# Kernel tuning notes

Hardware: AMD Instinct MI355X
Metric: run time of the kernel (lower is better)

Reference implementation:

```python
import jax, jax.numpy as jnp
import numpy as np
from jax import lax

THRESH = 0.6      # pnet score threshold (threshold[0])
IOU_THR = 0.5     # per-scale nms threshold in detect_face
K_PICKS = 128     # fixed max number of NMS picks (jit-static)
STRIDE = 2.0
CELL = 12.0
NEG = -1e30


def _conv(x, w, b):
    y = lax.conv_general_dilated(x, w, (1, 1), 'VALID',
                                 dimension_numbers=('NCHW', 'OIHW', 'NCHW'))
    return y + b[None, :, None, None]


def _prelu(x, a):
    return jnp.where(x > 0, x, a[None, :, None, None] * x)


def _maxpool2(x):
    return lax.reduce_window(x, -jnp.inf, lax.max, (1, 1, 2, 2), (1, 1, 2, 2), 'VALID')


def _nms(boxes, scores):
    # Greedy union-IoU NMS (nms_numpy math), vectorized with a fixed pick budget.
    # boxes [N,4] (shared grid), scores [N] with invalid entries already = NEG.
    x1, y1, x2, y2 = boxes[:, 0], boxes[:, 1], boxes[:, 2], boxes[:, 3]
    area = (x2 - x1 + 1.0) * (y2 - y1 + 1.0)

    def body(live, _):
        j = jnp.argmax(live)
        s = live[j]
        ok = s > NEG * 0.5
        xx1 = jnp.maximum(x1[j], x1); yy1 = jnp.maximum(y1[j], y1)
        xx2 = jnp.minimum(x2[j], x2); yy2 = jnp.minimum(y2[j], y2)
        inter = jnp.maximum(0.0, xx2 - xx1 + 1.0) * jnp.maximum(0.0, yy2 - yy1 + 1.0)
        iou = inter / (area[j] + area - inter)
        live = jnp.where(iou > IOU_THR, NEG, live).at[j].set(NEG)
        return live, (j, ok)

    _, (idx, ok) = lax.scan(body, scores, None, length=K_PICKS)
    return idx, ok


def setup_inputs():
    key = jax.random.key(0)
    ks = jax.random.split(key, 16)
    B, H, W = 16, 384, 512
    f = lambda k, shp, s=0.1: jax.random.normal(k, shp, jnp.float32) * s
    return {
        'im_data': jax.random.uniform(ks[0], (B, 3, H, W), jnp.float32) * 255.0,
        'c1_w': f(ks[1], (10, 3, 3, 3)), 'c1_b': f(ks[2], (10,)),
        'p1': jnp.full((10,), 0.25, jnp.float32),
        'c2_w': f(ks[3], (16, 10, 3, 3)), 'c2_b': f(ks[4], (16,)),
        'p2': jnp.full((16,), 0.25, jnp.float32),
        'c3_w': f(ks[5], (32, 16, 3, 3)), 'c3_b': f(ks[6], (32,)),
        'p3': jnp.full((32,), 0.25, jnp.float32),
        'c41_w': f(ks[7], (2, 32, 1, 1)), 'c41_b': f(ks[8], (2,)),
        'c42_w': f(ks[9], (4, 32, 1, 1)), 'c42_b': f(ks[10], (4,)),
    }


def reference(im_data, c1_w, c1_b, p1, c2_w, c2_b, p2, c3_w, c3_b, p3,
              c41_w, c41_b, c42_w, c42_b):
    # --- PNet conv trunk (detect_face normalization + MTCNN PNet) ---
    x = (im_data - 127.5) * 0.0078125
    h = _prelu(_conv(x, c1_w, c1_b), p1)
    h = _maxpool2(h)                                   # 2x2 s2 (dims even -> ceil==floor)
    h = _prelu(_conv(h, c2_w, c2_b), p2)
    h = _prelu(_conv(h, c3_w, c3_b), p3)
    probs = jax.nn.softmax(_conv(h, c41_w, c41_b), axis=1)[:, 1]   # [B,Hp,Wp]
    reg = _conv(h, c42_w, c42_b)                                   # [B,4,Hp,Wp]

    # --- generateBoundingBox (dense, masked instead of nonzero; scale=1) ---
    B, Hp, Wp = probs.shape
    yy, xx = jnp.meshgrid(jnp.arange(Hp, dtype=jnp.float32),
                          jnp.arange(Wp, dtype=jnp.float32), indexing='ij')
    boxes4 = jnp.stack([jnp.floor(STRIDE * xx + 1.0).ravel(),
                        jnp.floor(STRIDE * yy + 1.0).ravel(),
                        jnp.floor(STRIDE * xx + CELL).ravel(),
                        jnp.floor(STRIDE * yy + CELL).ravel()], axis=1)  # [N,4]
    scores = probs.reshape(B, -1)                                   # [B,N]
    regf = reg.reshape(B, 4, -1).transpose(0, 2, 1)                 # [B,N,4]
    masked = jnp.where(scores >= THRESH, scores, NEG)

    # --- per-image greedy NMS (batched_nms: images independent) ---
    idx, ok = jax.vmap(_nms, in_axes=(None, 0))(boxes4, masked)     # [B,K]
    pb = boxes4[idx]                                                # [B,K,4]
    ps = jnp.take_along_axis(scores, idx, axis=1)                   # [B,K]
    pr = jnp.take_along_axis(regf, idx[..., None], axis=1)          # [B,K,4]

    w = pb[..., 2] - pb[..., 0]
    hh = pb[..., 3] - pb[..., 1]
    q1 = pb[..., 0] + pr[..., 0] * w
    q2 = pb[..., 1] + pr[..., 1] * hh
    q3 = pb[..., 2] + pr[..., 2] * w
    q4 = pb[..., 3] + pr[..., 3] * hh
    rw = q3 - q1
    rh = q4 - q2
    l = jnp.maximum(rw, rh)
    nx1 = q1 + rw * 0.5 - l * 0.5
    ny1 = q2 + rh * 0.5 - l * 0.5
    out = jnp.stack([nx1, ny1, nx1 + l, ny1 + l, ps], axis=-1)      # [B,K,5]
    return out * ok[..., None].astype(out.dtype)
```

## Files before the change

### kernel.cpp

```cpp
#include <hip/hip_runtime.h>
#include <math.h>

#define BATCH 16
#define IH 384
#define IW 512
#define C1 10
#define P1H 191
#define P1W 255
#define C2 16
#define H2 189
#define W2 253
#define C3 32
#define H3 187
#define W3 251
#define N3 (H3*W3)
#define KP 128
#define CAP 7680
#define NEGV (-1e30f)

typedef _Float16 f16x8 __attribute__((ext_vector_type(8)));
typedef _Float16 f16x4 __attribute__((ext_vector_type(4)));
typedef float    f32x16 __attribute__((ext_vector_type(16)));

#define PXT 66
#define NSUB 2

#define T1R 34
#define T1C 68
__global__ __launch_bounds__(256, 1) void k_conv1pool(
        const float* __restrict__ im, const float* __restrict__ w,
        const float* __restrict__ bia, const float* __restrict__ slope,
        float* __restrict__ outp,
        const float* __restrict__ w3, _Float16* __restrict__ wbuf) {
    __shared__ float T[3 * T1R * T1C];

    int tx = threadIdx.x, ty = threadIdx.y;
    int tid = ty * 16 + tx;
    int bx = blockIdx.x, by = blockIdx.y, bb = blockIdx.z;

    if (bx == 0 && by == 0 && bb == 0) {
        for (int e = tid; e < 4608; e += 256) {
            int oc = e / 144;
            int rem = e - oc * 144;
            int ic = rem / 9;
            int tap = rem - ic * 9;
            float v = w3[e];
            _Float16 h = (_Float16)v;
            _Float16 l = (_Float16)(v - (float)h);
            int d = ((tap * 2 + (ic >> 3)) * 32 + oc) * 8 + (ic & 7);
            wbuf[d] = h;
            wbuf[4608 + d] = l;
        }
    }

    const size_t ibase = (size_t)bb * 3 * IH * IW;
    for (int g = tid; g < 3 * T1R * 33; g += 256) {
        int ch = g / (T1R * 33);
        int rem = g - ch * (T1R * 33);
        int r = rem / 33;
        int c2 = rem - r * 33;
        int yg = 32 * by + r;
        int xg = 64 * bx + 2 * c2;
        float2 v = make_float2(0.f, 0.f);
        if (yg < IH && xg < IW)
            v = *(const float2*)(im + ibase + ((size_t)ch * IH + yg) * IW + xg);
        float2 o;
        o.x = (v.x - 127.5f) * 0.0078125f;
        o.y = (v.y - 127.5f) * 0.0078125f;
        *(float2*)&T[(ch * T1R + r) * T1C + 2 * c2] = o;
    }
    __syncthreads();

    int Y  = by * 16 + ty;
    int X0 = bx * 32 + 2 * tx;
    if (Y >= P1H) return;

    float win[3][4][6];
    #pragma unroll
    for (int ch = 0; ch < 3; ++ch)
        #pragma unroll
        for (int r = 0; r < 4; ++r) {
            const float* p = &T[(ch * T1R + 2 * ty + r) * T1C + 4 * tx];
            float4 a = *(const float4*)p;
            float2 b = *(const float2*)(p + 4);
            win[ch][r][0] = a.x; win[ch][r][1] = a.y;
            win[ch][r][2] = a.z; win[ch][r][3] = a.w;
            win[ch][r][4] = b.x; win[ch][r][5] = b.y;
        }
    #pragma unroll
    for (int ch = 0; ch < 3; ++ch)
        #pragma unroll
        for (int r = 0; r < 4; ++r)
            #pragma unroll
            for (int c = 0; c < 6; ++c)
                asm volatile("" : "+v"(win[ch][r][c]));

    bool px1ok = (X0 + 1 < P1W);
    for (int oc = 0; oc < C1; ++oc) {
        const float* wo = w + oc * 27;
        float bv = bia[oc], sv = slope[oc];
        float c0 = bv, c1 = bv, c2 = bv, c3 = bv;
        float c4 = bv, c5 = bv, c6 = bv, c7 = bv;
        #pragma unroll
        for (int ch = 0; ch < 3; ++ch)
            #pragma unroll
            for (int ky = 0; ky < 3; ++ky)
                #pragma unroll
                for (int kx = 0; kx < 3; ++kx) {
                    float wv = wo[(ch * 3 + ky) * 3 + kx];
                    c0 += win[ch][0 + ky][0 + kx] * wv;
                    c1 += win[ch][0 + ky][1 + kx] * wv;
                    c2 += win[ch][0 + ky][2 + kx] * wv;
                    c3 += win[ch][0 + ky][3 + kx] * wv;
                    c4 += win[ch][1 + ky][0 + kx] * wv;
                    c5 += win[ch][1 + ky][1 + kx] * wv;
                    c6 += win[ch][1 + ky][2 + kx] * wv;
                    c7 += win[ch][1 + ky][3 + kx] * wv;
                }
        float m0 = fmaxf(fmaxf(c0, c1), fmaxf(c4, c5));
        float m1 = fmaxf(fmaxf(c2, c3), fmaxf(c6, c7));
        float p0 = m0 > 0.f ? m0 : sv * m0;
        float p1 = m1 > 0.f ? m1 : sv * m1;
        float* o = outp + (((size_t)bb * C1 + oc) * P1H + Y) * P1W + X0;
        o[0] = p0;
        if (px1ok) o[1] = p1;
    }
}

__global__ __launch_bounds__(256, 1) void k_conv2(
        const float* __restrict__ inp, const float* __restrict__ w,
        const float* __restrict__ bia, const float* __restrict__ slope,
        float* __restrict__ outp) {
    __shared__ __align__(16) float smem[8192];
    float* tile = smem;
    float4* sbuf = (float4*)smem;

    int tx = threadIdx.x, ty = threadIdx.y;
    int tid = ty * 64 + tx;
    int bx = blockIdx.x, byb = blockIdx.y, bb = blockIdx.z;

    const float* pin = inp + (size_t)bb * C1 * P1H * P1W;
    for (int g = tid; g < C1 * 6 * 130; g += 256) {
        int ic = g / 780;
        int rem = g - ic * 780;
        int r = rem / 130;
        int c = rem - r * 130;
        int yg = 4 * byb + r;
        int xg = 128 * bx + c;
        float v = 0.f;
        if (yg < P1H && xg < P1W)
            v = pin[((size_t)ic * P1H + yg) * P1W + xg];
        tile[(ic * 6 + r) * 132 + c] = v;
    }
    __syncthreads();

    int x0 = bx * 128 + tx * 2;
    int y  = byb * 4 + ty;
    bool alive = (x0 < W2) && (y < H2);

    float a0[C2], a1[C2];
    #pragma unroll
    for (int oc = 0; oc < C2; ++oc) { a0[oc] = bia[oc]; a1[oc] = bia[oc]; }

    if (alive) {
        #pragma unroll 1
        for (int ci = 0; ci < C1; ++ci) {
            float v[3][4];
            #pragma unroll
            for (int r = 0; r < 3; ++r) {
                const float* p = &tile[(ci * 6 + ty + r) * 132 + 2 * tx];
                float2 u0 = *(const float2*)p;
                float2 u1 = *(const float2*)(p + 2);
                v[r][0] = u0.x; v[r][1] = u0.y; v[r][2] = u1.x; v[r][3] = u1.y;
            }
            #pragma unroll
            for (int r = 0; r < 3; ++r)
                #pragma unroll
                for (int k = 0; k < 4; ++k)
                    asm volatile("" : "+v"(v[r][k]));
            const float* wc = w + ci * 9;
            #pragma unroll
            for (int oc = 0; oc < C2; ++oc) {
                const float* wo = wc + oc * (C1 * 9);
                float s0 = a0[oc], s1 = a1[oc];
                #pragma unroll
                for (int ky = 0; ky < 3; ++ky)
                    #pragma unroll
                    for (int kx = 0; kx < 3; ++kx) {
                        float wv = wo[ky * 3 + kx];
                        s0 += v[ky][kx]     * wv;
                        s1 += v[ky][kx + 1] * wv;
                    }
                a0[oc] = s0; a1[oc] = s1;
            }
        }
        #pragma unroll
        for (int oc = 0; oc < C2; ++oc) {
            float sl = slope[oc];
            float u0 = a0[oc]; a0[oc] = u0 > 0.f ? u0 : sl * u0;
            float u1 = a1[oc]; a1[oc] = u1 > 0.f ? u1 : sl * u1;
        }
    }
    __syncthreads();

    #pragma unroll
    for (int c4 = 0; c4 < 4; ++c4) {
        int g0 = tid * 8 + c4;
        int p0 = g0 ^ ((g0 >> 3) & 7);
        sbuf[p0] = make_float4(a0[c4 * 4], a0[c4 * 4 + 1], a0[c4 * 4 + 2], a0[c4 * 4 + 3]);
        int g1 = tid * 8 + 4 + c4;
        int p1 = g1 ^ ((g1 >> 3) & 7);
        sbuf[p1] = make_float4(a1[c4 * 4], a1[c4 * 4 + 1], a1[c4 * 4 + 2], a1[c4 * 4 + 3]);
    }
    __syncthreads();

    const size_t obase = (size_t)bb * H2 * W2 * C2;
    #pragma unroll
    for (int it = 0; it < 8; ++it) {
        int g = it * 256 + tid;
        int c4 = g & 3, px = (g >> 2) & 127, ry = g >> 9;
        int xg = bx * 128 + px, yg = byb * 4 + ry;
        if (xg < W2 && yg < H2) {
            int phys = g ^ ((g >> 3) & 7);
            *(float4*)(outp + obase + ((size_t)yg * W2 + xg) * C2 + c4 * 4) = sbuf[phys];
        }
    }
}

__global__ __launch_bounds__(256, 2) void k_conv3mfma(
        const float* __restrict__ act,
        const _Float16* __restrict__ wbuf,
        const float* __restrict__ b3, const float* __restrict__ s3,
        const float* __restrict__ w41, const float* __restrict__ b41,
        const float* __restrict__ w42, const float* __restrict__ b42,
        float* __restrict__ scores, float4* __restrict__ regf) {
    __shared__ __align__(16) _Float16 Ah[6 * 2 * PXT * 8];
    __shared__ __align__(16) _Float16 Al[6 * 2 * PXT * 8];
    __shared__ __align__(16) float    htab[32 * 8];

    int tid = threadIdx.x;
    int bx = blockIdx.x * (NSUB * 32);
    int by = blockIdx.y * 4;
    int bb = blockIdx.z;

    {
        int oc = tid >> 3, f = tid & 7;
        float v;
        if      (f == 0) v = b3[oc];
        else if (f == 1) v = s3[oc];
        else if (f == 2) v = w41[oc];
        else if (f == 3) v = w41[32 + oc];
        else             v = w42[(f - 4) * 32 + oc];
        htab[tid] = v;
    }
    {
        const float* actb = act + (size_t)bb * H2 * W2 * C2;
        for (int e = tid; e < 6 * PXT * 4; e += 256) {
            int ic4 = e & 3;
            int t = e >> 2;
            int px = t % PXT;
            int row = t / PXT;
            int yg = by + row, xg = bx + px;
            float4 v = make_float4(0.f, 0.f, 0.f, 0.f);
            if (yg < H2 && xg < W2)
                v = *(const float4*)(actb + ((size_t)yg * W2 + xg) * C2 + ic4 * 4);
            float xs0 = v.x, xs1 = v.y, xs2 = v.z, xs3 = v.w;
            f16x4 hv, lv;
            _Float16 h;
            h = (_Float16)xs0; hv[0] = h; lv[0] = (_Float16)(xs0 - (float)h);
            h = (_Float16)xs1; hv[1] = h; lv[1] = (_Float16)(xs1 - (float)h);
            h = (_Float16)xs2; hv[2] = h; lv[2] = (_Float16)(xs2 - (float)h);
            h = (_Float16)xs3; hv[3] = h; lv[3] = (_Float16)(xs3 - (float)h);
            int kg = ic4 >> 1, h4 = ic4 & 1;
            int gr = (row * 2 + kg) * PXT + px;
            *(f16x4*)(Ah + gr * 8 + h4 * 4) = hv;
            *(f16x4*)(Al + gr * 8 + h4 * 4) = lv;
        }
    }
    __syncthreads();

    int wv = tid >> 6, lane = tid & 63;
    int col = lane & 31, half = lane >> 5;
    int y = by + wv;
    if (y >= H3) return;

    f32x16 acc[NSUB];
    #pragma unroll
    for (int s = 0; s < NSUB; ++s)
        #pragma unroll
        for (int i = 0; i < 16; ++i) acc[s][i] = 0.f;

    const _Float16* wg = wbuf + (half * 32 + col) * 8;

    #pragma unroll 1
    for (int ky = 0; ky < 3; ++ky) {
        const _Float16* arh = Ah + ((wv + ky) * 2 + half) * (PXT * 8);
        const _Float16* arl = Al + ((wv + ky) * 2 + half) * (PXT * 8);
        #pragma unroll
        for (int kx = 0; kx < 3; ++kx) {
            int tap = ky * 3 + kx;
            f16x8 wh = *(const f16x8*)(wg + tap * 512);
            f16x8 wl = *(const f16x8*)(wg + 4608 + tap * 512);
            #pragma unroll
            for (int s = 0; s < NSUB; ++s) {
                int p = s * 32 + col + kx;
                f16x8 bh = *(const f16x8*)(arh + p * 8);
                f16x8 bl = *(const f16x8*)(arl + p * 8);
                acc[s] = __builtin_amdgcn_mfma_f32_32x32x16_f16(wh, bh, acc[s], 0, 0, 0);
                acc[s] = __builtin_amdgcn_mfma_f32_32x32x16_f16(wl, bh, acc[s], 0, 0, 0);
                acc[s] = __builtin_amdgcn_mfma_f32_32x32x16_f16(wh, bl, acc[s], 0, 0, 0);
            }
        }
    }

    float L0[NSUB], L1[NSUB], R0[NSUB], R1[NSUB], R2[NSUB], R3[NSUB];
    #pragma unroll
    for (int s = 0; s < NSUB; ++s) { L0[s]=0.f; L1[s]=0.f; R0[s]=0.f; R1[s]=0.f; R2[s]=0.f; R3[s]=0.f; }

    #pragma unroll
    for (int r = 0; r < 16; ++r) {
        int oc = (r & 3) + 8 * (r >> 2) + 4 * half;
        float4 t0 = *(const float4*)&htab[oc * 8];
        float4 t1 = *(const float4*)&htab[oc * 8 + 4];
        #pragma unroll
        for (int s = 0; s < NSUB; ++s) {
            float v = acc[s][r] + t0.x;
            v = v > 0.f ? v : v * t0.y;
            L0[s] += v * t0.z; L1[s] += v * t0.w;
            R0[s] += v * t1.x; R1[s] += v * t1.y;
            R2[s] += v * t1.z; R3[s] += v * t1.w;
        }
    }

    float hb0 = b41[0], hb1 = b41[1];
    float rb0 = b42[0], rb1 = b42[1], rb2 = b42[2], rb3 = b42[3];

    #pragma unroll
    for (int s = 0; s < NSUB; ++s) {
        float l0 = L0[s] + __shfl_xor(L0[s], 32) + hb0;
        float l1 = L1[s] + __shfl_xor(L1[s], 32) + hb1;
        float r0 = R0[s] + __shfl_xor(R0[s], 32) + rb0;
        float r1 = R1[s] + __shfl_xor(R1[s], 32) + rb1;
        float r2 = R2[s] + __shfl_xor(R2[s], 32) + rb2;
        float r3 = R3[s] + __shfl_xor(R3[s], 32) + rb3;
        float m = fmaxf(l0, l1);
        float e0 = expf(l0 - m), e1 = expf(l1 - m);
        float p = e1 / (e0 + e1);
        int px = bx + s * 32 + col;
        if (half == 0 && px < W3) {
            size_t n = (size_t)bb * N3 + (size_t)y * W3 + px;
            scores[n] = (p >= 0.6f) ? p : NEGV;
            regf[n] = make_float4(r0, r1, r2, r3);
        }
    }
}

__global__ __launch_bounds__(1024) void k_nms(
        const float* __restrict__ scores, const float4* __restrict__ regf,
        float* __restrict__ outp) {
    __shared__ float s_score[CAP];
    __shared__ int   s_idx[CAP];
    __shared__ float r_s[2][16];
    __shared__ int   r_i[2][16];
    __shared__ float s_picks[KP];
    __shared__ int   s_picki[KP];
    __shared__ int   s_misc[4];

    int tid = threadIdx.x;
    int bb = blockIdx.x;
    const float* sc = scores + (size_t)bb * N3;

    if (tid < 4) s_misc[tid] = 0;
    __syncthreads();

    int cnt = 0;
    for (int i = tid; i < N3; i += 1024) if (sc[i] > 0.f) cnt++;
    atomicAdd(&s_misc[0], cnt);
    __syncthreads();
    int M = s_misc[0];

    int cutbin = 0;
    if (M > CAP) {
        for (int i = tid; i < 2048; i += 1024) s_idx[i] = 0;
        __syncthreads();
        for (int i = tid; i < N3; i += 1024) {
            float s = sc[i];
            if (s > 0.f) {
                int b = (int)((s - 0.6f) * 5120.f);
                b = b < 0 ? 0 : (b > 2047 ? 2047 : b);
                atomicAdd(&s_idx[b], 1);
            }
        }
        __syncthreads();
        if (tid == 0) {
            int accum = 0, b = 2047;
            for (; b >= 0; --b) {
                int c = s_idx[b];
                if (accum + c > CAP) break;
                accum += c;
            }
            s_misc[2] = b + 1;
        }
        __syncthreads();
        cutbin = s_misc[2];
        __syncthreads();
    }

    for (int i = tid; i < N3; i += 1024) {
        float s = sc[i];
        if (s > 0.f) {
            bool keep = true;
            if (M > CAP) {
                int b = (int)((s - 0.6f) * 5120.f);
                b = b < 0 ? 0 : (b > 2047 ? 2047 : b);
                keep = (b >= cutbin);
            }
            if (keep) {
                int pos = atomicAdd(&s_misc[1], 1);
                if (pos < CAP) { s_score[pos] = s; s_idx[pos] = i; }
            }
        }
    }
    __syncthreads();
    int M2 = s_misc[1]; if (M2 > CAP) M2 = CAP;

    int np = 0;
    int   ppi = -1;
    float px1 = 0.f, py1 = 0.f, px2 = 0.f, py2 = 0.f;
    for (int pick = 0; pick < KP; ++pick) {
        float bs = -INFINITY; int bi = 0x7fffffff;
        for (int i = tid; i < M2; i += 1024) {
            float s = s_score[i];
            if (ppi >= 0 && s > NEGV * 0.5f) {
                int id = s_idx[i];
                int cx = id % W3, cy = id / W3;
                float x1 = (float)(2 * cx + 1), y1 = (float)(2 * cy + 1);
                float x2 = (float)(2 * cx + 12), y2 = (float)(2 * cy + 12);
                float xx1 = fmaxf(px1, x1), yy1 = fmaxf(py1, y1);
                float xx2 = fminf(px2, x2), yy2 = fminf(py2, y2);
                float inter = fmaxf(0.f, xx2 - xx1 + 1.f) * fmaxf(0.f, yy2 - yy1 + 1.f);
                float iou = inter / (288.f - inter);
                if (iou > 0.5f) { s = NEGV; s_score[i] = NEGV; }
            }
            int id = s_idx[i];
            if (s > bs || (s == bs && id < bi)) { bs = s; bi = id; }
        }
        #pragma unroll
        for (int off = 32; off; off >>= 1) {
            float os = __shfl_down(bs, off);
            int   oi = __shfl_down(bi, off);
            if (os > bs || (os == bs && oi < bi)) { bs = os; bi = oi; }
        }
        int lane = tid & 63, wv = tid >> 6, buf = pick & 1;
        if (lane == 0) { r_s[buf][wv] = bs; r_i[buf][wv] = bi; }
        __syncthreads();
        if (tid == 0) {
            float ps = r_s[buf][0]; int pi = r_i[buf][0];
            for (int k = 1; k < 16; ++k) {
                float os = r_s[buf][k]; int oi = r_i[buf][k];
                if (os > ps || (os == ps && oi < pi)) { ps = os; pi = oi; }
            }
            s_picks[pick] = ps; s_picki[pick] = pi;
            r_s[buf][0] = ps; r_i[buf][0] = pi;
        }
        __syncthreads();
        float ps = r_s[buf][0]; int pi = r_i[buf][0];
        if (ps < 0.f) break;
        np = pick + 1;

        ppi = pi;
        int pcx = pi % W3, pcy = pi / W3;
        px1 = (float)(2 * pcx + 1);  py1 = (float)(2 * pcy + 1);
        px2 = (float)(2 * pcx + 12); py2 = (float)(2 * pcy + 12);
    }

    if (tid < KP) {
        float* o = outp + ((size_t)bb * KP + tid) * 5;
        if (tid < np) {
            int pi = s_picki[tid]; float ps = s_picks[tid];
            int cx = pi % W3, cy = pi / W3;
            float x1 = (float)(2 * cx + 1), y1 = (float)(2 * cy + 1);
            float x2 = (float)(2 * cx + 12), y2 = (float)(2 * cy + 12);
            float4 r = regf[(size_t)bb * N3 + pi];
            float wd = x2 - x1, hh = y2 - y1;
            float q1 = x1 + r.x * wd, q2 = y1 + r.y * hh;
            float q3 = x2 + r.z * wd, q4 = y2 + r.w * hh;
            float rw = q3 - q1, rh = q4 - q2;
            float L = fmaxf(rw, rh);
            float nx1 = q1 + rw * 0.5f - L * 0.5f;
            float ny1 = q2 + rh * 0.5f - L * 0.5f;
            o[0] = nx1; o[1] = ny1; o[2] = nx1 + L; o[3] = ny1 + L; o[4] = ps;
        } else {
            o[0] = 0.f; o[1] = 0.f; o[2] = 0.f; o[3] = 0.f; o[4] = 0.f;
        }
    }
}

extern "C" void kernel_launch(void* const* d_in, const int* in_sizes, int n_in,
                              void* d_out, int out_size, void* d_ws, size_t ws_size,
                              hipStream_t stream) {
    const float* im   = (const float*)d_in[0];
    const float* c1w  = (const float*)d_in[1];
    const float* c1b  = (const float*)d_in[2];
    const float* p1   = (const float*)d_in[3];
    const float* c2w  = (const float*)d_in[4];
    const float* c2b  = (const float*)d_in[5];
    const float* p2   = (const float*)d_in[6];
    const float* c3w  = (const float*)d_in[7];
    const float* c3b  = (const float*)d_in[8];
    const float* p3   = (const float*)d_in[9];
    const float* c41w = (const float*)d_in[10];
    const float* c41b = (const float*)d_in[11];
    const float* c42w = (const float*)d_in[12];
    const float* c42b = (const float*)d_in[13];

    float* ws = (float*)d_ws;
    const size_t POOL1_FLOATS = (size_t)BATCH * C1 * P1H * P1W;
    float*  pool1  = ws;
    float*  conv2b = ws + POOL1_FLOATS;
    float*  scoresb = ws;
    float4* regfb   = (float4*)(ws + (size_t)BATCH * N3);
    _Float16* wbuf = (_Float16*)d_out;

    k_conv1pool<<<dim3(8, 12, BATCH), dim3(16, 16), 0, stream>>>(im, c1w, c1b, p1, pool1,
                                                                 c3w, wbuf);
    k_conv2   <<<dim3(2, 48, BATCH), dim3(64, 4), 0, stream>>>(pool1, c2w, c2b, p2, conv2b);
    k_conv3mfma<<<dim3(4, 47, BATCH), dim3(256), 0, stream>>>(conv2b, wbuf, c3b, p3,
                                                              c41w, c41b, c42w, c42b,
                                                              scoresb, regfb);
    k_nms<<<dim3(BATCH), dim3(1024), 0, stream>>>(scoresb, regfb, (float*)d_out);
}
```

Baseline: 250.0 us.

## Read conv2 input directly from padded global rows; halve NMS block and drop serial reduce

```diff
diff --git a/kernel.cpp b/kernel.cpp
--- a/kernel.cpp
+++ b/kernel.cpp
@@ -7,6 +7,7 @@
 #define C1 10
 #define P1H 191
 #define P1W 255
+#define P1S 256
 #define C2 16
 #define H2 189
 #define W2 253
@@ -121,109 +122,72 @@
         float m1 = fmaxf(fmaxf(c2, c3), fmaxf(c6, c7));
         float p0 = m0 > 0.f ? m0 : sv * m0;
         float p1 = m1 > 0.f ? m1 : sv * m1;
-        float* o = outp + (((size_t)bb * C1 + oc) * P1H + Y) * P1W + X0;
+        float* o = outp + (((size_t)bb * C1 + oc) * P1H + Y) * P1S + X0;
         o[0] = p0;
         if (px1ok) o[1] = p1;
     }
 }
 
-__global__ __launch_bounds__(256, 1) void k_conv2(
+__global__ __launch_bounds__(256, 2) void k_conv2(
         const float* __restrict__ inp, const float* __restrict__ w,
         const float* __restrict__ bia, const float* __restrict__ slope,
         float* __restrict__ outp) {
-    __shared__ __align__(16) float smem[8192];
-    float* tile = smem;
-    float4* sbuf = (float4*)smem;
-
-    int tx = threadIdx.x, ty = threadIdx.y;
-    int tid = ty * 64 + tx;
-    int bx = blockIdx.x, byb = blockIdx.y, bb = blockIdx.z;
-
-    const float* pin = inp + (size_t)bb * C1 * P1H * P1W;
-    for (int g = tid; g < C1 * 6 * 130; g += 256) {
-        int ic = g / 780;
-        int rem = g - ic * 780;
-        int r = rem / 130;
-        int c = rem - r * 130;
-        int yg = 4 * byb + r;
-        int xg = 128 * bx + c;
-        float v = 0.f;
-        if (yg < P1H && xg < P1W)
-            v = pin[((size_t)ic * P1H + yg) * P1W + xg];
-        tile[(ic * 6 + r) * 132 + c] = v;
-    }
-    __syncthreads();
-
-    int x0 = bx * 128 + tx * 2;
-    int y  = byb * 4 + ty;
-    bool alive = (x0 < W2) && (y < H2);
+    int x0 = (blockIdx.x * 64 + threadIdx.x) * 2;
+    int y  = blockIdx.y * 4 + threadIdx.y;
+    int bb = blockIdx.z;
+    if (x0 >= W2 || y >= H2) return;
 
     float a0[C2], a1[C2];
     #pragma unroll
     for (int oc = 0; oc < C2; ++oc) { a0[oc] = bia[oc]; a1[oc] = bia[oc]; }
 
-    if (alive) {
-        #pragma unroll 1
-        for (int ci = 0; ci < C1; ++ci) {
-            float v[3][4];
+    bool tail = (x0 + 3 > P1W - 1);
+
+    for (int ci = 0; ci < C1; ++ci) {
+        const float* p = inp + (((size_t)bb * C1 + ci) * P1H + y) * P1S + x0;
+        float v[3][4];
+        #pragma unroll
+        for (int r = 0; r < 3; ++r) {
+            const float* pr = p + (size_t)r * P1S;
+            float2 u0 = *(const float2*)pr;
+            float2 u1 = *(const float2*)(pr + 2);
+            v[r][0] = u0.x; v[r][1] = u0.y; v[r][2] = u1.x;
+            v[r][3] = tail ? 0.f : u1.y;
+        }
+        const float* wc = w + ci * 9;
+        #pragma unroll
+        for (int oc = 0; oc < C2; ++oc) {
+            const float* wo = wc + oc * (C1 * 9);
+            float s0 = a0[oc], s1 = a1[oc];
             #pragma unroll
-            for (int r = 0; r < 3; ++r) {
-                const float* p = &tile[(ci * 6 + ty + r) * 132 + 2 * tx];
-                float2 u0 = *(const float2*)p;
-                float2 u1 = *(const float2*)(p + 2);
-                v[r][0] = u0.x; v[r][1] = u0.y; v[r][2] = u1.x; v[r][3] = u1.y;
-            }
-            #pragma unroll
-            for (int r = 0; r < 3; ++r)
+            for (int ky = 0; ky < 3; ++ky)
                 #pragma unroll
-                for (int k = 0; k < 4; ++k)
-                    asm volatile("" : "+v"(v[r][k]));
-            const float* wc = w + ci * 9;
-            #pragma unroll
-            for (int oc = 0; oc < C2; ++oc) {
-                const float* wo = wc + oc * (C1 * 9);
-                float s0 = a0[oc], s1 = a1[oc];
-                #pragma unroll
-                for (int ky = 0; ky < 3; ++ky)
-                    #pragma unroll
-                    for (int kx = 0; kx < 3; ++kx) {
-                        float wv = wo[ky * 3 + kx];
-                        s0 += v[ky][kx]     * wv;
-                        s1 += v[ky][kx + 1] * wv;
-                    }
-                a0[oc] = s0; a1[oc] = s1;
-            }
-        }
-        #pragma unroll
-        for (int oc = 0; oc < C2; ++oc) {
-            float sl = slope[oc];
-            float u0 = a0[oc]; a0[oc] = u0 > 0.f ? u0 : sl * u0;
-            float u1 = a1[oc]; a1[oc] = u1 > 0.f ? u1 : sl * u1;
-        }
-    }
-    __syncthreads();
-
-    #pragma unroll
-    for (int c4 = 0; c4 < 4; ++c4) {
-        int g0 = tid * 8 + c4;
-        int p0 = g0 ^ ((g0 >> 3) & 7);
-        sbuf[p0] = make_float4(a0[c4 * 4], a0[c4 * 4 + 1], a0[c4 * 4 + 2], a0[c4 * 4 + 3]);
-        int g1 = tid * 8 + 4 + c4;
-        int p1 = g1 ^ ((g1 >> 3) & 7);
-        sbuf[p1] = make_float4(a1[c4 * 4], a1[c4 * 4 + 1], a1[c4 * 4 + 2], a1[c4 * 4 + 3]);
-    }
-    __syncthreads();
-
-    const size_t obase = (size_t)bb * H2 * W2 * C2;
-    #pragma unroll
-    for (int it = 0; it < 8; ++it) {
-        int g = it * 256 + tid;
-        int c4 = g & 3, px = (g >> 2) & 127, ry = g >> 9;
-        int xg = bx * 128 + px, yg = byb * 4 + ry;
-        if (xg < W2 && yg < H2) {
-            int phys = g ^ ((g >> 3) & 7);
-            *(float4*)(outp + obase + ((size_t)yg * W2 + xg) * C2 + c4 * 4) = sbuf[phys];
-        }
+                for (int kx = 0; kx < 3; ++kx) {
+                    float wv = wo[ky * 3 + kx];
+                    s0 += v[ky][kx]     * wv;
+                    s1 += v[ky][kx + 1] * wv;
+                }
+            a0[oc] = s0; a1[oc] = s1;
+        }
+    }
+    #pragma unroll
+    for (int oc = 0; oc < C2; ++oc) {
+        float sl = slope[oc];
+        float u0 = a0[oc]; a0[oc] = u0 > 0.f ? u0 : sl * u0;
+        float u1 = a1[oc]; a1[oc] = u1 > 0.f ? u1 : sl * u1;
+    }
+    float* o = outp + (((size_t)bb * H2 + y) * W2 + x0) * C2;
+    float4* o4 = (float4*)o;
+    o4[0] = make_float4(a0[0],  a0[1],  a0[2],  a0[3]);
+    o4[1] = make_float4(a0[4],  a0[5],  a0[6],  a0[7]);
+    o4[2] = make_float4(a0[8],  a0[9],  a0[10], a0[11]);
+    o4[3] = make_float4(a0[12], a0[13], a0[14], a0[15]);
+    if (x0 + 1 < W2) {
+        float4* p4 = (float4*)(o + C2);
+        p4[0] = make_float4(a1[0],  a1[1],  a1[2],  a1[3]);
+        p4[1] = make_float4(a1[4],  a1[5],  a1[6],  a1[7]);
+        p4[2] = make_float4(a1[8],  a1[9],  a1[10], a1[11]);
+        p4[3] = make_float4(a1[12], a1[13], a1[14], a1[15]);
     }
 }
 
@@ -355,13 +319,13 @@
     }
 }
 
-__global__ __launch_bounds__(1024) void k_nms(
+__global__ __launch_bounds__(512) void k_nms(
         const float* __restrict__ scores, const float4* __restrict__ regf,
         float* __restrict__ outp) {
     __shared__ float s_score[CAP];
     __shared__ int   s_idx[CAP];
-    __shared__ float r_s[2][16];
-    __shared__ int   r_i[2][16];
+    __shared__ float r_s[2][8];
+    __shared__ int   r_i[2][8];
     __shared__ float s_picks[KP];
     __shared__ int   s_picki[KP];
     __shared__ int   s_misc[4];
@@ -374,16 +338,16 @@
     __syncthreads();
 
     int cnt = 0;
-    for (int i = tid; i < N3; i += 1024) if (sc[i] > 0.f) cnt++;
+    for (int i = tid; i < N3; i += 512) if (sc[i] > 0.f) cnt++;
     atomicAdd(&s_misc[0], cnt);
     __syncthreads();
     int M = s_misc[0];
 
     int cutbin = 0;
     if (M > CAP) {
-        for (int i = tid; i < 2048; i += 1024) s_idx[i] = 0;
+        for (int i = tid; i < 2048; i += 512) s_idx[i] = 0;
         __syncthreads();
-        for (int i = tid; i < N3; i += 1024) {
+        for (int i = tid; i < N3; i += 512) {
             float s = sc[i];
             if (s > 0.f) {
                 int b = (int)((s - 0.6f) * 5120.f);
@@ -406,7 +370,7 @@
         __syncthreads();
     }
 
-    for (int i = tid; i < N3; i += 1024) {
+    for (int i = tid; i < N3; i += 512) {
         float s = sc[i];
         if (s > 0.f) {
             bool keep = true;
@@ -429,7 +393,7 @@
     float px1 = 0.f, py1 = 0.f, px2 = 0.f, py2 = 0.f;
     for (int pick = 0; pick < KP; ++pick) {
         float bs = -INFINITY; int bi = 0x7fffffff;
-        for (int i = tid; i < M2; i += 1024) {
+        for (int i = tid; i < M2; i += 512) {
             float s = s_score[i];
             if (ppi >= 0 && s > NEGV * 0.5f) {
                 int id = s_idx[i];
@@ -454,18 +418,14 @@
         int lane = tid & 63, wv = tid >> 6, buf = pick & 1;
         if (lane == 0) { r_s[buf][wv] = bs; r_i[buf][wv] = bi; }
         __syncthreads();
-        if (tid == 0) {
-            float ps = r_s[buf][0]; int pi = r_i[buf][0];
-            for (int k = 1; k < 16; ++k) {
-                float os = r_s[buf][k]; int oi = r_i[buf][k];
-                if (os > ps || (os == ps && oi < pi)) { ps = os; pi = oi; }
-            }
-            s_picks[pick] = ps; s_picki[pick] = pi;
-            r_s[buf][0] = ps; r_i[buf][0] = pi;
-        }
-        __syncthreads();
         float ps = r_s[buf][0]; int pi = r_i[buf][0];
+        #pragma unroll
+        for (int k = 1; k < 8; ++k) {
+            float os = r_s[buf][k]; int oi = r_i[buf][k];
+            if (os > ps || (os == ps && oi < pi)) { ps = os; pi = oi; }
+        }
         if (ps < 0.f) break;
+        if (tid == 0) { s_picks[pick] = ps; s_picki[pick] = pi; }
         np = pick + 1;
 
         ppi = pi;
@@ -473,6 +433,7 @@
         px1 = (float)(2 * pcx + 1);  py1 = (float)(2 * pcy + 1);
         px2 = (float)(2 * pcx + 12); py2 = (float)(2 * pcy + 12);
     }
+    __syncthreads();
 
     if (tid < KP) {
         float* o = outp + ((size_t)bb * KP + tid) * 5;
@@ -515,9 +476,9 @@
     const float* c42b = (const float*)d_in[13];
 
     float* ws = (float*)d_ws;
-    const size_t POOL1_FLOATS = (size_t)BATCH * C1 * P1H * P1W;
-    float*  pool1  = ws;
-    float*  conv2b = ws + POOL1_FLOATS;
+    const size_t P1FLOATS = (size_t)BATCH * C1 * P1H * P1S;
+    float*  pool1   = ws;
+    float*  conv2b  = ws + P1FLOATS;
     float*  scoresb = ws;
     float4* regfb   = (float4*)(ws + (size_t)BATCH * N3);
     _Float16* wbuf = (_Float16*)d_out;
@@ -528,5 +489,5 @@
     k_conv3mfma<<<dim3(4, 47, BATCH), dim3(256), 0, stream>>>(conv2b, wbuf, c3b, p3,
                                                               c41w, c41b, c42w, c42b,
                                                               scoresb, regfb);
-    k_nms<<<dim3(BATCH), dim3(1024), 0, stream>>>(scoresb, regfb, (float*)d_out);
+    k_nms<<<dim3(BATCH), dim3(512), 0, stream>>>(scoresb, regfb, (float*)d_out);
 }
```

Result: faster. 244.0 us (-2.4%).
